# Kernel optimization log

Hardware: AMD Instinct MI355X
Metric: run time of the kernel (lower is better)

## Reference

```python
import jax, jax.numpy as jnp
import numpy as np

# ---- static config (from init_kwargs) ----
UP = 2
DOWN = 2
NEG_SLOPE = 0.2
MARGIN = 10
FLRELU_SCALE = np.float32(2.0 ** 0.5)  # fused_leaky_relu default scale
# p = K - factor = 12 - 2 = 10; padding=True branch
UP_PAD = ((10 + 1) // 2 + UP - 1, 10 // 2)      # (6, 5)
DOWN_PAD = ((10 + 1) // 2, 10 // 2)             # (5, 5)

# 12-tap hann-windowed-sinc lowpass (sum normalized to 1), as in alias-free GAN
_FILT = np.array([0.0, 0.00398, -0.01884, -0.05155, 0.12443, 0.44197,
                  0.44197, 0.12443, -0.05155, -0.01884, 0.00398, 0.0],
                 dtype=np.float32)
_FILT = _FILT / _FILT.sum()


def _fir1d(x, k, up, down, pad0, pad1, axis):
    """upfirdn along one spatial axis of NCHW x with 1D kernel k.

    Matches upfirdn2d_native: zero-stuff by `up` (including up-1 trailing
    zeros, folded into right padding), pad, correlate with flipped kernel
    (= FIR convolution), stride-`down` subsample.
    """
    N, C, H, W = x.shape
    xr = x.reshape(N * C, 1, H, W)
    K = k.shape[0]
    kf = k[::-1].astype(x.dtype)  # flip -> true convolution, as in native op
    if axis == 3:  # width
        w = kf.reshape(1, 1, 1, K)
        lhs_dil = (1, up)
        strides = (1, down)
        padding = ((0, 0), (pad0, pad1 + up - 1))
    else:          # height
        w = kf.reshape(1, 1, K, 1)
        lhs_dil = (up, 1)
        strides = (down, 1)
        padding = ((pad0, pad1 + up - 1), (0, 0))
    y = jax.lax.conv_general_dilated(
        xr, w, window_strides=strides, padding=padding,
        lhs_dilation=lhs_dil, dimension_numbers=('NCHW', 'OIHW', 'NCHW'))
    return y.reshape(N, C, y.shape[2], y.shape[3])


def _sep_upfirdn(x, k, up, down, pad):
    # module applies the separable 1D filter along width first, then height,
    # with the same (pad0, pad1) on each axis
    x = _fir1d(x, k, up, down, pad[0], pad[1], axis=3)
    x = _fir1d(x, k, up, down, pad[0], pad[1], axis=2)
    return x


def setup_inputs() -> dict:
    key = jax.random.key(0)
    k_in = jax.random.fold_in(key, 0)
    return {
        'input': jax.random.normal(k_in, (8, 512, 64, 64), dtype=jnp.float32),
        'bias': jnp.zeros((512,), dtype=jnp.float32),
        'up_filter': jnp.asarray(_FILT),
        'down_filter': jnp.asarray(_FILT),
    }


def reference(input, bias, up_filter, down_filter):
    out = input + bias[None, :, None, None]
    # 1D upsample filter is pre-scaled by the upsample factor at init
    upf = up_filter * UP
    out = _sep_upfirdn(out, upf, UP, 1, UP_PAD)          # 64 -> 128
    out = jax.nn.leaky_relu(out, NEG_SLOPE) * FLRELU_SCALE
    out = _sep_upfirdn(out, down_filter, 1, DOWN, DOWN_PAD)  # 128 -> 64
    m = (MARGIN * UP - MARGIN * DOWN) // 2
    if m > 0:
        out = out[:, :, m:-m, m:-m]
    return out
```

## Files before the change

kernel.cpp:

```cpp
#include <hip/hip_runtime.h>

#define TPB 512
#define H 64
#define W 64

#define NT1 72
#define T1S 132
#define T1_FLOATS (NT1 * T1S)
#define T2S 140
#define T2_OFF 4
#define LDS_FLOATS T1_FLOATS

typedef float v2f __attribute__((ext_vector_type(2)));

#define PKF_ACC_P(acc,a,b)  asm("v_pk_fma_f32 %0, %1, %2, %0 op_sel:[0,0,0] op_sel_hi:[1,1,1]" : "+v"(acc) : "v"(a), "v"(b))
#define PKF_ACC_A0(acc,a,b) asm("v_pk_fma_f32 %0, %1, %2, %0 op_sel:[0,0,0] op_sel_hi:[0,1,1]" : "+v"(acc) : "v"(a), "v"(b))
#define PKF_ACC_A1(acc,a,b) asm("v_pk_fma_f32 %0, %1, %2, %0 op_sel:[1,0,0] op_sel_hi:[1,1,1]" : "+v"(acc) : "v"(a), "v"(b))
#define PKF_ACC_B0(acc,a,b) asm("v_pk_fma_f32 %0, %1, %2, %0 op_sel:[0,0,0] op_sel_hi:[1,0,1]" : "+v"(acc) : "v"(a), "v"(b))
#define PKF_ACC_B1(acc,a,b) asm("v_pk_fma_f32 %0, %1, %2, %0 op_sel:[0,1,0] op_sel_hi:[1,1,1]" : "+v"(acc) : "v"(a), "v"(b))
#define PKF_NEW_B0(d,a,b,c) asm("v_pk_fma_f32 %0, %1, %2, %3 op_sel:[0,0,0] op_sel_hi:[1,0,1]" : "=v"(d) : "v"(a), "v"(b), "v"(c))
#define PKF_NEW_B1(d,a,b,c) asm("v_pk_fma_f32 %0, %1, %2, %3 op_sel:[0,1,0] op_sel_hi:[1,1,1]" : "=v"(d) : "v"(a), "v"(b), "v"(c))
#define PKM_P(d,a,b)        asm("v_pk_mul_f32 %0, %1, %2 op_sel:[0,0] op_sel_hi:[1,1]" : "=v"(d) : "v"(a), "v"(b))
#define PKM_A0(d,a,b)       asm("v_pk_mul_f32 %0, %1, %2 op_sel:[0,0] op_sel_hi:[0,1]" : "=v"(d) : "v"(a), "v"(b))
#define PKM_A1(d,a,b)       asm("v_pk_mul_f32 %0, %1, %2 op_sel:[1,0] op_sel_hi:[1,1]" : "=v"(d) : "v"(a), "v"(b))
#define PKM_B0(d,a,b)       asm("v_pk_mul_f32 %0, %1, %2 op_sel:[0,0] op_sel_hi:[1,0]" : "=v"(d) : "v"(a), "v"(b))

__global__ __launch_bounds__(TPB, 6)
void afa_fused(const float* __restrict__ in, const float* __restrict__ bias,
               const float* __restrict__ upf, const float* __restrict__ dnf,
               float* __restrict__ out)
{
    __shared__ __align__(16) float lds[LDS_FLOATS];
    float* const s_t1 = lds;
    float* const s_t2 = lds;

    const int tid = threadIdx.x;
    const int plane = blockIdx.x;

    v2f gp[5], fh[5], fdp[5];
#pragma unroll
    for (int k = 0; k < 5; ++k) {
        gp[k]  = (v2f){2.0f * upf[9 - 2*k], 2.0f * upf[10 - 2*k]};
        fh[k]  = (v2f){1.41421356237309515f * dnf[2*k + 1], 1.41421356237309515f * dnf[2*k + 2]};
        fdp[k] = (v2f){dnf[10 - 2*k], dnf[9 - 2*k]};
    }
    const float bv = bias[plane & 511];
    const v2f b2  = (v2f){bv, bv};
    const v2f cst = (v2f){0.6f, 0.4f};
    const v2f z2  = (v2f){0.f, 0.f};

    if (tid < 264) {
        *(float2*)(s_t1 + 2 * tid) = make_float2(0.f, 0.f);
        *(float2*)(s_t1 + 68 * T1S + 2 * tid) = make_float2(0.f, 0.f);
    }

    {
        const int r  = tid >> 3;
        const int cb = tid & 7;
        const float4* p4 = (const float4*)(in + (size_t)plane * (H * W) + r * W);
        float4 q0 = p4[cb == 0 ? 0 : 2 * cb - 1];
        const float4 q1 = p4[2 * cb];
        const float4 q2 = p4[2 * cb + 1];
        float4 q3 = p4[cb == 7 ? 15 : 2 * cb + 2];
        if (cb == 0) q0 = make_float4(0.f, 0.f, 0.f, 0.f);
        if (cb == 7) q3 = make_float4(0.f, 0.f, 0.f, 0.f);
        v2f wr2[6];
        wr2[0] = (v2f){q0.z, q0.w};
        wr2[1] = (v2f){q1.x, q1.y};  wr2[2] = (v2f){q1.z, q1.w};
        wr2[3] = (v2f){q2.x, q2.y};  wr2[4] = (v2f){q2.z, q2.w};
        wr2[5] = (v2f){q3.x, q3.y};
        v2f po[8];
#pragma unroll
        for (int q = 0; q < 8; ++q) {
            if (q & 1) { PKM_A1(po[q], wr2[q >> 1], gp[0]); }
            else       { PKM_A0(po[q], wr2[q >> 1], gp[0]); }
#pragma unroll
            for (int k = 1; k < 5; ++k) {
                if ((q + k) & 1) { PKF_ACC_A1(po[q], wr2[(q + k) >> 1], gp[k]); }
                else             { PKF_ACC_A0(po[q], wr2[(q + k) >> 1], gp[k]); }
            }
        }
        float* dst = s_t1 + (r + 4) * T1S + 16 * cb;
#pragma unroll
        for (int k = 0; k < 4; ++k)
            *(float4*)(dst + 4 * k) = make_float4(po[2*k][0], po[2*k][1], po[2*k+1][0], po[2*k+1][1]);
    }
    __syncthreads();

    const int c = tid & 63;
    const int q = tid >> 6;
    v2f accp[8] = {z2, z2, z2, z2, z2, z2, z2, z2};
    {
        v2f cc[16];
#pragma unroll
        for (int t = 0; t < 16; ++t)
            cc[t] = *(const v2f*)(s_t1 + (8 * q + t) * T1S + 2 * c);
        const bool mlo = (q == 0);
        const bool mhi = (q == 7);
#pragma unroll
        for (int t = 0; t < 12; ++t) {
            v2f ta, tb;
            PKF_NEW_B0(ta, cc[t], gp[0], b2);
            PKF_NEW_B1(tb, cc[t], gp[0], b2);
#pragma unroll
            for (int k = 1; k < 5; ++k) {
                PKF_ACC_B0(ta, cc[t + k], gp[k]);
                PKF_ACC_B1(tb, cc[t + k], gp[k]);
            }
            if (mlo && t < 2)   { ta = z2; tb = z2; }
            if (mhi && t >= 10) { ta = z2; tb = z2; }
            v2f ra, aa, rb, ab;
            PKM_B0(ra, ta, cst);
            aa[0] = __builtin_fabsf(ta[0]); aa[1] = __builtin_fabsf(ta[1]);
            PKF_ACC_B1(ra, aa, cst);
            PKM_B0(rb, tb, cst);
            ab[0] = __builtin_fabsf(tb[0]); ab[1] = __builtin_fabsf(tb[1]);
            PKF_ACC_B1(rb, ab, cst);
#pragma unroll
            for (int p = 0; p < 8; ++p) {
                if (p <= t && t <= p + 4) {
                    const int m = 4 - (t - p);
                    PKF_ACC_B1(accp[p], ra, fh[m]);
                    PKF_ACC_B0(accp[p], rb, fh[m]);
                }
            }
        }
    }
    __syncthreads();

#pragma unroll
    for (int p = 0; p < 8; ++p)
        *(v2f*)(s_t2 + (8 * q + p) * T2S + T2_OFF + 2 * c) = accp[p];
    {
        const int rw = tid >> 3, cz = tid & 7;
        s_t2[rw * T2S + (cz < 4 ? cz : 128 + cz)] = 0.f;
    }
    __syncthreads();

#pragma unroll
    for (int s_ = 0; s_ < 2; ++s_) {
        const int u = tid + 512 * s_;
        const int oy = u >> 4, oxb = u & 15;
        const float* base = s_t2 + oy * T2S + 8 * oxb;
        v2f Wp[8];
#pragma unroll
        for (int j = 0; j < 8; ++j) Wp[j] = *(const v2f*)(base + 2 * j);
        float o2[4];
#pragma unroll
        for (int p = 0; p < 4; ++p) {
            v2f acc;
            PKM_P(acc, Wp[p], fdp[0]);
#pragma unroll
            for (int m = 1; m < 5; ++m)
                PKF_ACC_P(acc, Wp[p + m], fdp[m]);
            o2[p] = acc[0] + acc[1];
        }
        float* po = out + (size_t)plane * (H * W) + oy * W + 4 * oxb;
        *(float4*)po = make_float4(o2[0], o2[1], o2[2], o2[3]);
    }
}

extern "C" void kernel_launch(void* const* d_in, const int* in_sizes, int n_in,
                              void* d_out, int out_size, void* d_ws, size_t ws_size,
                              hipStream_t stream) {
    const float* in  = (const float*)d_in[0];
    const float* bv  = (const float*)d_in[1];
    const float* upf = (const float*)d_in[2];
    const float* dnf = (const float*)d_in[3];
    float* out = (float*)d_out;
    afa_fused<<<8 * 512, TPB, 0, stream>>>(in, bv, upf, dnf, out);
}
```

Baseline: 40.49 us.

## Compute horizontal upsample FIR with bf16 MFMA instead of packed FMAs

Replaces the first-stage horizontal upsampling FIR, previously done with packed fp32 FMAs per thread, with a banded-matrix multiply on the matrix cores via mfma_f32_16x16x32_bf16. Inputs and filter taps are converted to bf16 and the upsampled rows are scattered into LDS from the MFMA accumulator layout. This is meant to offload ALU work from the first stage, at the cost of bf16 precision loss, clamped, partly redundant global loads, and scalar strided LDS stores.

```diff
diff --git a/kernel.cpp b/kernel.cpp
--- a/kernel.cpp
+++ b/kernel.cpp
@@ -12,17 +12,22 @@
 #define LDS_FLOATS T1_FLOATS
 
 typedef float v2f __attribute__((ext_vector_type(2)));
+typedef float f32x4 __attribute__((ext_vector_type(4)));
+typedef short s16x8 __attribute__((ext_vector_type(8)));
+typedef unsigned int u32;
+typedef u32 u32x4 __attribute__((ext_vector_type(4)));
+union FR { u32x4 u; s16x8 s; };
+
+__device__ __forceinline__ u32 pkbf(float lo, float hi) {
+    u32 d; asm("v_cvt_pk_bf16_f32 %0, %1, %2" : "=v"(d) : "v"(lo), "v"(hi)); return d;
+}
 
 #define PKF_ACC_P(acc,a,b)  asm("v_pk_fma_f32 %0, %1, %2, %0 op_sel:[0,0,0] op_sel_hi:[1,1,1]" : "+v"(acc) : "v"(a), "v"(b))
-#define PKF_ACC_A0(acc,a,b) asm("v_pk_fma_f32 %0, %1, %2, %0 op_sel:[0,0,0] op_sel_hi:[0,1,1]" : "+v"(acc) : "v"(a), "v"(b))
-#define PKF_ACC_A1(acc,a,b) asm("v_pk_fma_f32 %0, %1, %2, %0 op_sel:[1,0,0] op_sel_hi:[1,1,1]" : "+v"(acc) : "v"(a), "v"(b))
 #define PKF_ACC_B0(acc,a,b) asm("v_pk_fma_f32 %0, %1, %2, %0 op_sel:[0,0,0] op_sel_hi:[1,0,1]" : "+v"(acc) : "v"(a), "v"(b))
 #define PKF_ACC_B1(acc,a,b) asm("v_pk_fma_f32 %0, %1, %2, %0 op_sel:[0,1,0] op_sel_hi:[1,1,1]" : "+v"(acc) : "v"(a), "v"(b))
 #define PKF_NEW_B0(d,a,b,c) asm("v_pk_fma_f32 %0, %1, %2, %3 op_sel:[0,0,0] op_sel_hi:[1,0,1]" : "=v"(d) : "v"(a), "v"(b), "v"(c))
 #define PKF_NEW_B1(d,a,b,c) asm("v_pk_fma_f32 %0, %1, %2, %3 op_sel:[0,1,0] op_sel_hi:[1,1,1]" : "=v"(d) : "v"(a), "v"(b), "v"(c))
 #define PKM_P(d,a,b)        asm("v_pk_mul_f32 %0, %1, %2 op_sel:[0,0] op_sel_hi:[1,1]" : "=v"(d) : "v"(a), "v"(b))
-#define PKM_A0(d,a,b)       asm("v_pk_mul_f32 %0, %1, %2 op_sel:[0,0] op_sel_hi:[0,1]" : "=v"(d) : "v"(a), "v"(b))
-#define PKM_A1(d,a,b)       asm("v_pk_mul_f32 %0, %1, %2 op_sel:[1,0] op_sel_hi:[1,1]" : "=v"(d) : "v"(a), "v"(b))
 #define PKM_B0(d,a,b)       asm("v_pk_mul_f32 %0, %1, %2 op_sel:[0,0] op_sel_hi:[1,0]" : "=v"(d) : "v"(a), "v"(b))
 
 __global__ __launch_bounds__(TPB, 6)
@@ -55,35 +60,48 @@
     }
 
     {
-        const int r  = tid >> 3;
-        const int cb = tid & 7;
-        const float4* p4 = (const float4*)(in + (size_t)plane * (H * W) + r * W);
-        float4 q0 = p4[cb == 0 ? 0 : 2 * cb - 1];
-        const float4 q1 = p4[2 * cb];
-        const float4 q2 = p4[2 * cb + 1];
-        float4 q3 = p4[cb == 7 ? 15 : 2 * cb + 2];
-        if (cb == 0) q0 = make_float4(0.f, 0.f, 0.f, 0.f);
-        if (cb == 7) q3 = make_float4(0.f, 0.f, 0.f, 0.f);
-        v2f wr2[6];
-        wr2[0] = (v2f){q0.z, q0.w};
-        wr2[1] = (v2f){q1.x, q1.y};  wr2[2] = (v2f){q1.z, q1.w};
-        wr2[3] = (v2f){q2.x, q2.y};  wr2[4] = (v2f){q2.z, q2.w};
-        wr2[5] = (v2f){q3.x, q3.y};
-        v2f po[8];
+        const int lane = tid & 63, w = tid >> 6;
+        const int lm = lane & 15, lg = lane >> 4;
+        const int u0 = 8 * (w & ~1) - 8;
+        FR uhf;
+        {
+            u32 fu[4];
+            const int i = 16 * w + lm;
 #pragma unroll
-        for (int q = 0; q < 8; ++q) {
-            if (q & 1) { PKM_A1(po[q], wr2[q >> 1], gp[0]); }
-            else       { PKM_A0(po[q], wr2[q >> 1], gp[0]); }
+            for (int pr = 0; pr < 4; ++pr) {
+                float h_[2];
 #pragma unroll
-            for (int k = 1; k < 5; ++k) {
-                if ((q + k) & 1) { PKF_ACC_A1(po[q], wr2[(q + k) >> 1], gp[k]); }
-                else             { PKF_ACC_A0(po[q], wr2[(q + k) >> 1], gp[k]); }
+                for (int hh = 0; hh < 2; ++hh) {
+                    const int uu = u0 + 8 * lg + 2 * pr + hh;
+                    const int d = i + 5 - 2 * uu;
+                    const int dc = (d < 0) ? 0 : (d > 11 ? 11 : d);
+                    const bool ok = (uu >= 0) && (uu <= 63) && (d >= 1) && (d <= 10);
+                    h_[hh] = ok ? 2.0f * upf[dc] : 0.f;
+                }
+                fu[pr] = pkbf(h_[0], h_[1]);
             }
+            uhf.u = (u32x4){fu[0], fu[1], fu[2], fu[3]};
         }
-        float* dst = s_t1 + (r + 4) * T1S + 16 * cb;
+        const f32x4 z4f = {0.f, 0.f, 0.f, 0.f};
+        const float* xp = in + (size_t)plane * (H * W);
 #pragma unroll
-        for (int k = 0; k < 4; ++k)
-            *(float4*)(dst + 4 * k) = make_float4(po[2*k][0], po[2*k][1], po[2*k+1][0], po[2*k+1][1]);
+        for (int mt = 0; mt < 4; ++mt) {
+            const int r = 16 * mt + lm;
+            const int us = u0 + 8 * lg;
+            const int q1 = us < 0 ? 0 : (us > 60 ? 60 : us);
+            const int uq = us + 4;
+            const int q2 = uq < 0 ? 0 : (uq > 60 ? 60 : uq);
+            const f32x4 a0 = *(const f32x4*)(xp + r * 64 + q1);
+            const f32x4 a1 = *(const f32x4*)(xp + r * 64 + q2);
+            FR af;
+            af.u = (u32x4){pkbf(a0.x, a0.y), pkbf(a0.z, a0.w),
+                           pkbf(a1.x, a1.y), pkbf(a1.z, a1.w)};
+            f32x4 c = __builtin_amdgcn_mfma_f32_16x16x32_bf16(af.s, uhf.s, z4f, 0, 0, 0);
+            float* dst = s_t1 + (16 * mt + 4 * lg + 4) * T1S + 16 * w + lm;
+#pragma unroll
+            for (int reg = 0; reg < 4; ++reg)
+                dst[reg * T1S] = c[reg];
+        }
     }
     __syncthreads();
 
```

Result: slower. 52.62 us (+30.0%).
